# Optimization experiments

Measured on AMD Instinct MI355X. Metric: run time of the kernel, lower is better.

## Reference

```python
import jax, jax.numpy as jnp
import numpy as np

NUM_HEADS = 8
WINDOW = 7
DILATION = 1
EPS = 1e-5


def channel_ln(x, w, b):
    # x: [B, C, H, W]; normalize over channel dim (axis=1)
    mu = jnp.mean(x, axis=1, keepdims=True)
    var = jnp.var(x, axis=1, keepdims=True)
    xhat = (x - mu) * jax.lax.rsqrt(var + EPS)
    return xhat * w[None, :, None, None] + b[None, :, None, None]


def local_mask(H, W, window, dilation):
    r = (window // 2) * dilation
    ii, jj = jnp.meshgrid(jnp.arange(H), jnp.arange(W), indexing="ij")
    ii = ii.reshape(-1)
    jj = jj.reshape(-1)
    di = jnp.abs(ii[:, None] - ii[None, :])
    dj = jnp.abs(jj[:, None] - jj[None, :])
    m = (di <= r) & (dj <= r)
    if dilation > 1:
        m = m & (di % dilation == 0) & (dj % dilation == 0)
    return m  # [N, N] bool


def local_attention(x, qkv_w, qkv_b, proj_w, proj_b):
    B, C, H, W = x.shape
    N = H * W
    hd = C // NUM_HEADS
    t = x.reshape(B, C, N).transpose(0, 2, 1)            # [B, N, C]
    qkv = t @ qkv_w.T + qkv_b                            # [B, N, 3C]
    qkv = qkv.reshape(B, N, 3, NUM_HEADS, hd)
    q, k, v = (qkv[:, :, i].transpose(0, 2, 1, 3) for i in range(3))  # [B,h,N,d]
    scale = 1.0 / jnp.sqrt(jnp.asarray(hd, x.dtype))
    scores = jnp.einsum("bhnd,bhmd->bhnm", q, k) * scale  # [B,h,N,N]
    mask = local_mask(H, W, WINDOW, DILATION)             # [N,N]
    scores = jnp.where(mask[None, None], scores, jnp.asarray(-jnp.inf, x.dtype))
    attn = jax.nn.softmax(scores, axis=-1)
    out = jnp.einsum("bhnm,bhmd->bhnd", attn, v)          # [B,h,N,d]
    out = out.transpose(0, 2, 1, 3).reshape(B, N, C)      # [B,N,C]
    out = out @ proj_w.T + proj_b
    return out.transpose(0, 2, 1).reshape(B, C, H, W)


def mlp2d(x, fc1_w, fc1_b, fc2_w, fc2_b):
    # 1x1 convs == per-pixel linear over channels
    h = jnp.einsum("bchw,oc->bohw", x, fc1_w) + fc1_b[None, :, None, None]
    h = jax.nn.gelu(h, approximate=False)
    return jnp.einsum("bchw,oc->bohw", h, fc2_w) + fc2_b[None, :, None, None]


def setup_inputs() -> dict:
    key = jax.random.key(0)
    ks = jax.random.split(key, 12)
    B, C, H, W = 1, 256, 56, 56
    hidden = 4 * C
    s = lambda fan: 1.0 / np.sqrt(fan)
    return {
        "x": jax.random.normal(ks[0], (B, C, H, W), jnp.float32),
        "norm1_w": jnp.ones((C,), jnp.float32),
        "norm1_b": jnp.zeros((C,), jnp.float32),
        "qkv_w": jax.random.normal(ks[1], (3 * C, C), jnp.float32) * s(C),
        "qkv_b": jnp.zeros((3 * C,), jnp.float32),
        "proj_w": jax.random.normal(ks[2], (C, C), jnp.float32) * s(C),
        "proj_b": jnp.zeros((C,), jnp.float32),
        "norm2_w": jnp.ones((C,), jnp.float32),
        "norm2_b": jnp.zeros((C,), jnp.float32),
        "fc1_w": jax.random.normal(ks[3], (hidden, C), jnp.float32) * s(C),
        "fc1_b": jnp.zeros((hidden,), jnp.float32),
        "fc2_w": jax.random.normal(ks[4], (C, hidden), jnp.float32) * s(hidden),
        "fc2_b": jnp.zeros((C,), jnp.float32),
    }


def reference(x, norm1_w, norm1_b, qkv_w, qkv_b, proj_w, proj_b,
              norm2_w, norm2_b, fc1_w, fc1_b, fc2_w, fc2_b):
    x = x + local_attention(channel_ln(x, norm1_w, norm1_b), qkv_w, qkv_b, proj_w, proj_b)
    x = x + mlp2d(channel_ln(x, norm2_w, norm2_b), fc1_w, fc1_b, fc2_w, fc2_b)
    return x
```

## Files before the change

### kernel.cpp

```cpp
#include <hip/hip_runtime.h>
#include <math.h>


typedef unsigned int uint;
typedef unsigned short ushort;
typedef unsigned long long u64;
typedef __attribute__((ext_vector_type(8))) short short8;
typedef __attribute__((ext_vector_type(4))) float floatx4;
typedef __attribute__((ext_vector_type(4))) unsigned short ushort4v;

#define AS1(p) (const __attribute__((address_space(1))) void*)(p)
#define AS3(p) (__attribute__((address_space(3))) void*)(p)

__device__ __forceinline__ float bf2f(ushort u) {
  union { uint i; float f; } v; v.i = ((uint)u) << 16; return v.f;
}
__device__ __forceinline__ ushort f2bf(float f) {
  union { float f; uint i; } v; v.f = f;
  uint u = v.i;
  return (ushort)((u + 0x7fffu + ((u >> 16) & 1u)) >> 16);
}

__device__ __forceinline__ void stage64(const ushort* src, int kstride,
                                        ushort* dstBase, int tid) {
  const int srow = tid >> 5;
  const int scb  = (tid & 31) ^ srow;
  const ushort* g = src + (size_t)srow * kstride + scb * 8;
  ushort* d = dstBase + tid * 8;
  #pragma unroll
  for (int r = 0; r < 8; ++r) {
    __builtin_amdgcn_global_load_lds(AS1(g), AS3(d), 16, 0, 0);
    g += 8 * kstride;
    d += 2048;
  }
}

__device__ __forceinline__ void compute64(const ushort* As, const ushort* Bs,
                                          int w, int lane, floatx4 acc[4]) {
  const int fm = lane & 15;
  const int q  = lane >> 4;
  const int swz = fm & 7;
  const int arow = (w * 16 + fm) * 256;
  #pragma unroll
  for (int kt = 0; kt < 8; ++kt) {
    const int blk = ((kt * 4 + q) ^ swz) * 8;
    short8 af = *(const short8*)&As[arow + blk];
    #pragma unroll
    for (int nt = 0; nt < 4; ++nt) {
      short8 bfr = *(const short8*)&Bs[(nt * 16 + fm) * 256 + blk];
      acc[nt] = __builtin_amdgcn_mfma_f32_16x16x32_bf16(af, bfr, acc[nt], 0, 0, 0);
    }
  }
}

__global__ __launch_bounds__(256) void prep_kernel(
    const float* __restrict__ x, const float* __restrict__ n1w,
    const float* __restrict__ n1b,
    const float* __restrict__ qkvw, const float* __restrict__ projw,
    const float* __restrict__ f1w, const float* __restrict__ f2w,
    float* __restrict__ xT, ushort* __restrict__ t1, ushort* __restrict__ wcat)
{
  const int tid = threadIdx.x;
  const int bid = blockIdx.x;
  if (bid >= 196) {
    int idx = (bid - 196) * 256 + tid;
    float v;
    if (idx < 196608)       v = qkvw[idx];
    else if (idx < 262144)  v = projw[idx - 196608];
    else if (idx < 524288)  v = f1w[idx - 262144];
    else                    v = f2w[idx - 524288];
    wcat[idx] = f2bf(v);
    return;
  }
  __shared__ float tile[256 * 17];
  __shared__ float red[2][16][16];
  __shared__ float mu[16], rsv[16];
  const int n0 = bid * 16;
  const int px = tid & 15, grp = tid >> 4;
  #pragma unroll 4
  for (int it = 0; it < 16; ++it) {
    int c = it * 16 + grp;
    tile[c * 17 + px] = x[(size_t)c * 3136 + n0 + px];
  }
  __syncthreads();
  float s = 0.f, ss = 0.f;
  #pragma unroll
  for (int i = 0; i < 16; ++i) {
    float v = tile[(grp * 16 + i) * 17 + px];
    s += v; ss += v * v;
  }
  red[0][px][grp] = s; red[1][px][grp] = ss;
  __syncthreads();
  if (tid < 16) {
    float s2 = 0.f, ss2 = 0.f;
    #pragma unroll
    for (int g = 0; g < 16; ++g) { s2 += red[0][tid][g]; ss2 += red[1][tid][g]; }
    float m = s2 * (1.f / 256.f);
    float var = ss2 * (1.f / 256.f) - m * m;
    mu[tid] = m;
    rsv[tid] = rsqrtf(var + 1e-5f);
  }
  __syncthreads();
  const float wc = n1w[tid], bc = n1b[tid];
  #pragma unroll 4
  for (int p = 0; p < 16; ++p) {
    float v = tile[tid * 17 + p];
    xT[(size_t)(n0 + p) * 256 + tid] = v;
    t1[(size_t)(n0 + p) * 256 + tid] = f2bf((v - mu[p]) * rsv[p] * wc + bc);
  }
}

__global__ __launch_bounds__(256, 2) void qkv_kernel(
    const ushort* __restrict__ A, const ushort* __restrict__ B,
    const float* __restrict__ bias, ushort* __restrict__ out)
{
  __shared__ ushort As[16384], Bs[16384];
  const int tid = threadIdx.x, lane = tid & 63, w = tid >> 6;
  const int m0 = blockIdx.y * 64, n0 = blockIdx.x * 64;
  floatx4 acc[4] = {{0.f,0.f,0.f,0.f},{0.f,0.f,0.f,0.f},
                    {0.f,0.f,0.f,0.f},{0.f,0.f,0.f,0.f}};
  stage64(A + (size_t)m0 * 256, 256, As, tid);
  stage64(B + (size_t)n0 * 256, 256, Bs, tid);
  asm volatile("s_waitcnt vmcnt(0)" ::: "memory");
  __syncthreads();
  compute64(As, Bs, w, lane, acc);
  const int fm = lane & 15, q4 = (lane >> 4) * 4;
  #pragma unroll
  for (int nt = 0; nt < 4; ++nt)
    #pragma unroll
    for (int r = 0; r < 4; ++r) {
      int m = m0 + w * 16 + q4 + r;
      int n = n0 + nt * 16 + fm;
      float v = acc[nt][r] + bias[n];
      if (n < 256) v *= 0.17677669529663687f;
      out[(size_t)m * 768 + n] = f2bf(v);
    }
}

__global__ __launch_bounds__(256, 1) void attn_kernel(
    const ushort* __restrict__ qkv, ushort* __restrict__ out)
{
  __shared__ ushort Kh[100 * 260];
  __shared__ ushort Vh[100 * 256];
  __shared__ float pr[16 * 8 * 64];
  const int tid = threadIdx.x;
  const int i0 = (blockIdx.x / 14) * 4, j0 = (blockIdx.x % 14) * 4;

  for (int s = tid; s < 3200; s += 256) {
    int p = s >> 5, ck = s & 31;
    int ii = i0 - 3 + p / 10, jj = j0 - 3 + p % 10;
    if (ii >= 0 && ii < 56 && jj >= 0 && jj < 56) {
      const ushort* kr = qkv + (size_t)(ii * 56 + jj) * 768 + 256 + ck * 8;
      short8 kv = *(const short8*)kr;
      u64 lo = ((const u64*)&kv)[0], hi = ((const u64*)&kv)[1];
      *(u64*)&Kh[p * 260 + ck * 8] = lo;
      *(u64*)&Kh[p * 260 + ck * 8 + 4] = hi;
      *(short8*)&Vh[p * 256 + ck * 8] = *(const short8*)(kr + 256);
    } else {
      *(u64*)&Kh[p * 260 + ck * 8] = 0ull;
      *(u64*)&Kh[p * 260 + ck * 8 + 4] = 0ull;
      short8 z = {0, 0, 0, 0, 0, 0, 0, 0};
      *(short8*)&Vh[p * 256 + ck * 8] = z;
    }
  }
  __syncthreads();

  const int wv = tid >> 6, lane = tid & 63;
  const int h = lane >> 3, mg = lane & 7;
  for (int qq = 0; qq < 4; ++qq) {
    const int p = wv * 4 + qq;
    const int qi = p >> 2, qj = p & 3;
    const int iq = i0 + qi, jq = j0 + qj;
    const ushort* qp = qkv + (size_t)(iq * 56 + jq) * 768 + h * 32;
    float qf[32];
    #pragma unroll
    for (int u = 0; u < 4; ++u) {
      short8 qv = *(const short8*)(qp + u * 8);
      #pragma unroll
      for (int e = 0; e < 8; ++e) qf[u * 8 + e] = bf2f((ushort)qv[e]);
    }
    float sv[7];
    float mx = -1e30f;
    #pragma unroll
    for (int k = 0; k < 7; ++k) {
      int m = mg + 8 * k;
      float s = -1e30f;
      if (m < 49) {
        int mi = m / 7, mj = m % 7;
        int ii = iq + mi - 3, jj = jq + mj - 3;
        if (ii >= 0 && ii < 56 && jj >= 0 && jj < 56) {
          int hrow = (qi + mi) * 10 + (qj + mj);
          const u64* k8 = (const u64*)&Kh[hrow * 260 + h * 32];
          float a = 0.f;
          #pragma unroll
          for (int u = 0; u < 8; ++u) {
            u64 kv = k8[u];
            #pragma unroll
            for (int e = 0; e < 4; ++e)
              a += qf[u * 4 + e] * bf2f((ushort)(kv >> (16 * e)));
          }
          s = a;
        }
      }
      sv[k] = s;
      mx = fmaxf(mx, s);
    }
    mx = fmaxf(mx, __shfl_xor(mx, 1));
    mx = fmaxf(mx, __shfl_xor(mx, 2));
    mx = fmaxf(mx, __shfl_xor(mx, 4));
    float sm = 0.f;
    #pragma unroll
    for (int k = 0; k < 7; ++k) { sv[k] = __expf(sv[k] - mx); sm += sv[k]; }
    sm += __shfl_xor(sm, 1);
    sm += __shfl_xor(sm, 2);
    sm += __shfl_xor(sm, 4);
    float inv = 1.f / sm;
    #pragma unroll
    for (int k = 0; k < 7; ++k) {
      int m = mg + 8 * k;
      pr[(p * 8 + h) * 64 + m] = sv[k] * inv;
    }
  }
  __syncthreads();

  const int qsel = tid >> 5, cg = tid & 31, hh = cg >> 2;
  #pragma unroll
  for (int pass = 0; pass < 2; ++pass) {
    const int p = pass * 8 + qsel;
    const int qi = p >> 2, qj = p & 3;
    float acc8[8] = {0, 0, 0, 0, 0, 0, 0, 0};
    #pragma unroll
    for (int mi = 0; mi < 7; ++mi)
      #pragma unroll
      for (int mj = 0; mj < 7; ++mj) {
        int m = mi * 7 + mj;
        int hrow = (qi + mi) * 10 + (qj + mj);
        float pm = pr[(p * 8 + hh) * 64 + m];
        short8 v8 = *(const short8*)&Vh[hrow * 256 + cg * 8];
        #pragma unroll
        for (int e = 0; e < 8; ++e)
          acc8[e] += pm * bf2f((ushort)v8[e]);
      }
    const int n = (i0 + qi) * 56 + (j0 + qj);
    short8 o;
    #pragma unroll
    for (int e = 0; e < 8; ++e) o[e] = (short)f2bf(acc8[e]);
    *(short8*)&out[(size_t)n * 256 + cg * 8] = o;
  }
}

__global__ __launch_bounds__(256, 2) void proj_kernel(
    const ushort* __restrict__ A, const ushort* __restrict__ B,
    const float* __restrict__ bias, const float* __restrict__ resid,
    float* __restrict__ x1)
{
  __shared__ ushort As[16384], Bs[16384];
  const int tid = threadIdx.x, lane = tid & 63, w = tid >> 6;
  const int m0 = blockIdx.y * 64, n0 = blockIdx.x * 64;
  floatx4 acc[4] = {{0.f,0.f,0.f,0.f},{0.f,0.f,0.f,0.f},
                    {0.f,0.f,0.f,0.f},{0.f,0.f,0.f,0.f}};
  stage64(A + (size_t)m0 * 256, 256, As, tid);
  stage64(B + (size_t)n0 * 256, 256, Bs, tid);
  asm volatile("s_waitcnt vmcnt(0)" ::: "memory");
  __syncthreads();
  compute64(As, Bs, w, lane, acc);
  const int fm = lane & 15, q4 = (lane >> 4) * 4;
  #pragma unroll
  for (int nt = 0; nt < 4; ++nt)
    #pragma unroll
    for (int r = 0; r < 4; ++r) {
      int m = m0 + w * 16 + q4 + r;
      int n = n0 + nt * 16 + fm;
      x1[(size_t)m * 256 + n] = acc[nt][r] + bias[n] + resid[(size_t)m * 256 + n];
    }
}

__global__ __launch_bounds__(256, 2) void fc1_kernel(
    const float* __restrict__ x1, const ushort* __restrict__ B,
    const float* __restrict__ n2w, const float* __restrict__ n2b,
    const float* __restrict__ bias, ushort* __restrict__ out)
{
  __shared__ ushort As[16384], Bs[16384];
  __shared__ float stats[128];
  const int tid = threadIdx.x, lane = tid & 63, w = tid >> 6;
  const int m0 = blockIdx.y * 64, n0 = blockIdx.x * 64;

  stage64(B + (size_t)n0 * 256, 256, Bs, tid);

  {
    const int r = tid >> 2, seg = tid & 3;
    const float* src = x1 + (size_t)(m0 + r) * 256 + seg * 64;
    float s = 0.f, ss = 0.f;
    #pragma unroll
    for (int i = 0; i < 16; ++i) {
      floatx4 v = *(const floatx4*)(src + i * 4);
      s += v[0] + v[1] + v[2] + v[3];
      ss += v[0]*v[0] + v[1]*v[1] + v[2]*v[2] + v[3]*v[3];
    }
    s += __shfl_xor(s, 1); ss += __shfl_xor(ss, 1);
    s += __shfl_xor(s, 2); ss += __shfl_xor(ss, 2);
    if (seg == 0) {
      float mu = s * (1.f / 256.f);
      float var = ss * (1.f / 256.f) - mu * mu;
      stats[r * 2] = mu;
      stats[r * 2 + 1] = rsqrtf(var + 1e-5f);
    }
  }
  __syncthreads();
  #pragma unroll
  for (int k = 0; k < 8; ++k) {
    int s = tid + k * 256;
    int row = s >> 5, cb = s & 31;
    int gb = cb ^ (row & 7);
    float mu = stats[row * 2], rs = stats[row * 2 + 1];
    const float* src = x1 + (size_t)(m0 + row) * 256 + gb * 8;
    floatx4 a = *(const floatx4*)(src);
    floatx4 b2 = *(const floatx4*)(src + 4);
    floatx4 w1 = *(const floatx4*)(n2w + gb * 8);
    floatx4 w2 = *(const floatx4*)(n2w + gb * 8 + 4);
    floatx4 b1v = *(const floatx4*)(n2b + gb * 8);
    floatx4 b2v = *(const floatx4*)(n2b + gb * 8 + 4);
    short8 o;
    #pragma unroll
    for (int e = 0; e < 4; ++e) {
      o[e]     = (short)f2bf((a[e]  - mu) * rs * w1[e] + b1v[e]);
      o[e + 4] = (short)f2bf((b2[e] - mu) * rs * w2[e] + b2v[e]);
    }
    *(short8*)&As[row * 256 + cb * 8] = o;
  }
  asm volatile("s_waitcnt vmcnt(0)" ::: "memory");
  __syncthreads();

  floatx4 acc[4] = {{0.f,0.f,0.f,0.f},{0.f,0.f,0.f,0.f},
                    {0.f,0.f,0.f,0.f},{0.f,0.f,0.f,0.f}};
  compute64(As, Bs, w, lane, acc);
  const int fm = lane & 15, q4 = (lane >> 4) * 4;
  #pragma unroll
  for (int nt = 0; nt < 4; ++nt)
    #pragma unroll
    for (int r = 0; r < 4; ++r) {
      int m = m0 + w * 16 + q4 + r;
      int n = n0 + nt * 16 + fm;
      float v = acc[nt][r] + bias[n];
      v = 0.5f * v * (1.0f + erff(v * 0.70710678118654752f));
      out[(size_t)m * 1024 + n] = f2bf(v);
    }
}

__global__ __launch_bounds__(256, 2) void fc2_kernel(
    const ushort* __restrict__ A, const ushort* __restrict__ B,
    const float* __restrict__ bias, const float* __restrict__ x1,
    float* __restrict__ outf)
{
  __shared__ ushort As[16384], Bs[16384];
  const int tid = threadIdx.x, lane = tid & 63, w = tid >> 6;
  const int m0 = blockIdx.y * 64, n0 = blockIdx.x * 64;
  floatx4 acc[4] = {{0.f,0.f,0.f,0.f},{0.f,0.f,0.f,0.f},
                    {0.f,0.f,0.f,0.f},{0.f,0.f,0.f,0.f}};
  for (int kc = 0; kc < 4; ++kc) {
    if (kc) __syncthreads();
    stage64(A + (size_t)m0 * 1024 + kc * 256, 1024, As, tid);
    stage64(B + (size_t)n0 * 1024 + kc * 256, 1024, Bs, tid);
    asm volatile("s_waitcnt vmcnt(0)" ::: "memory");
    __syncthreads();
    compute64(As, Bs, w, lane, acc);
  }
  const int fm = lane & 15, q4 = (lane >> 4) * 4;
  #pragma unroll
  for (int nt = 0; nt < 4; ++nt)
    #pragma unroll
    for (int r = 0; r < 4; ++r) {
      int m = m0 + w * 16 + q4 + r;
      int n = n0 + nt * 16 + fm;
      outf[(size_t)m * 3136 + n] = acc[nt][r] + bias[m] + x1[(size_t)n * 256 + m];
    }
}

extern "C" void kernel_launch(void* const* d_in, const int* in_sizes, int n_in,
                              void* d_out, int out_size, void* d_ws, size_t ws_size,
                              hipStream_t stream) {
  const float* x     = (const float*)d_in[0];
  const float* n1w   = (const float*)d_in[1];
  const float* n1b   = (const float*)d_in[2];
  const float* qkvw  = (const float*)d_in[3];
  const float* qkvb  = (const float*)d_in[4];
  const float* projw = (const float*)d_in[5];
  const float* projb = (const float*)d_in[6];
  const float* n2w   = (const float*)d_in[7];
  const float* n2b   = (const float*)d_in[8];
  const float* f1w   = (const float*)d_in[9];
  const float* f1b   = (const float*)d_in[10];
  const float* f2w   = (const float*)d_in[11];
  const float* f2b   = (const float*)d_in[12];

  char* ws = (char*)d_ws;
  ushort* wcat = (ushort*)(ws + 0);
  float*  xT   = (float*)(ws + 1572864);
  ushort* t    = (ushort*)(ws + 4784128);
  ushort* qh   = (ushort*)(ws + 6389760);
  ushort* attnO= (ushort*)(ws + 12812288);

  const ushort* qw_bf = wcat;
  const ushort* pw_bf = wcat + 196608;
  const ushort* f1_bf = wcat + 262144;
  const ushort* f2_bf = wcat + 524288;
  float* outf = (float*)d_out;

  hipLaunchKernelGGL(prep_kernel, dim3(3268), dim3(256), 0, stream,
                     x, n1w, n1b, qkvw, projw, f1w, f2w, xT, t, wcat);
  hipLaunchKernelGGL(qkv_kernel, dim3(12, 49), dim3(256), 0, stream,
                     t, qw_bf, qkvb, qh);
  hipLaunchKernelGGL(attn_kernel, dim3(196), dim3(256), 0, stream, qh, attnO);
  hipLaunchKernelGGL(proj_kernel, dim3(4, 49), dim3(256), 0, stream,
                     attnO, pw_bf, projb, xT, xT);
  hipLaunchKernelGGL(fc1_kernel, dim3(16, 49), dim3(256), 0, stream,
                     xT, f1_bf, n2w, n2b, f1b, qh);
  hipLaunchKernelGGL(fc2_kernel, dim3(49, 4), dim3(256), 0, stream,
                     f2_bf, qh, f2b, xT, outf);
}
```

Baseline: 147.0 us.

## Fuse output projection and residual add into the local attention kernel

The attention kernel now keeps its 16-query by 256-channel output tile in shared memory and applies the output projection directly. It streams the projection weights through double-buffered shared-memory chunks that reuse the dead K and probability regions, then does MFMA plus bias and residual add. This removes the separate proj launch and the global write and read of the attention output. The cost is that every block now reads the full projection weight matrix for only 16 rows, which adds L2 traffic. The result also goes to a new x1 buffer instead of being written back into xT.

```diff
diff --git a/kernel.cpp b/kernel.cpp
--- a/kernel.cpp
+++ b/kernel.cpp
@@ -137,12 +137,21 @@
     }
 }
 
-__global__ __launch_bounds__(256, 1) void attn_kernel(
-    const ushort* __restrict__ qkv, ushort* __restrict__ out)
+#define ATTN_SMEM 144416
+
+__global__ __launch_bounds__(256, 1) void attnproj_kernel(
+    const ushort* __restrict__ qkv, const ushort* __restrict__ pw_bf,
+    const float* __restrict__ projb, const float* __restrict__ xT,
+    float* __restrict__ x1)
 {
-  __shared__ ushort Kh[100 * 260];
-  __shared__ ushort Vh[100 * 256];
-  __shared__ float pr[16 * 8 * 64];
+  __shared__ __align__(16) char smem[ATTN_SMEM];
+  ushort* Kh  = (ushort*)smem;
+  ushort* Vh  = (ushort*)(smem + 52000);
+  float*  pr  = (float*)(smem + 103200);
+  ushort* aas = (ushort*)(smem + 135968);
+  ushort* Bs0 = (ushort*)smem;
+  ushort* Bs1 = (ushort*)(smem + 103200);
+
   const int tid = threadIdx.x;
   const int i0 = (blockIdx.x / 14) * 4, j0 = (blockIdx.x % 14) * 4;
 
@@ -223,56 +232,62 @@
   }
   __syncthreads();
 
-  const int qsel = tid >> 5, cg = tid & 31, hh = cg >> 2;
-  #pragma unroll
-  for (int pass = 0; pass < 2; ++pass) {
-    const int p = pass * 8 + qsel;
-    const int qi = p >> 2, qj = p & 3;
-    float acc8[8] = {0, 0, 0, 0, 0, 0, 0, 0};
-    #pragma unroll
-    for (int mi = 0; mi < 7; ++mi)
+  stage64(pw_bf, 256, Bs0, tid);
+
+  {
+    const int qsel = tid >> 5, cg = tid & 31, hh = cg >> 2;
+    #pragma unroll
+    for (int pass = 0; pass < 2; ++pass) {
+      const int p = pass * 8 + qsel;
+      const int qi = p >> 2, qj = p & 3;
+      float acc8[8] = {0, 0, 0, 0, 0, 0, 0, 0};
       #pragma unroll
-      for (int mj = 0; mj < 7; ++mj) {
-        int m = mi * 7 + mj;
-        int hrow = (qi + mi) * 10 + (qj + mj);
-        float pm = pr[(p * 8 + hh) * 64 + m];
-        short8 v8 = *(const short8*)&Vh[hrow * 256 + cg * 8];
+      for (int mi = 0; mi < 7; ++mi)
         #pragma unroll
-        for (int e = 0; e < 8; ++e)
-          acc8[e] += pm * bf2f((ushort)v8[e]);
-      }
-    const int n = (i0 + qi) * 56 + (j0 + qj);
-    short8 o;
-    #pragma unroll
-    for (int e = 0; e < 8; ++e) o[e] = (short)f2bf(acc8[e]);
-    *(short8*)&out[(size_t)n * 256 + cg * 8] = o;
-  }
-}
-
-__global__ __launch_bounds__(256, 2) void proj_kernel(
-    const ushort* __restrict__ A, const ushort* __restrict__ B,
-    const float* __restrict__ bias, const float* __restrict__ resid,
-    float* __restrict__ x1)
-{
-  __shared__ ushort As[16384], Bs[16384];
-  const int tid = threadIdx.x, lane = tid & 63, w = tid >> 6;
-  const int m0 = blockIdx.y * 64, n0 = blockIdx.x * 64;
-  floatx4 acc[4] = {{0.f,0.f,0.f,0.f},{0.f,0.f,0.f,0.f},
-                    {0.f,0.f,0.f,0.f},{0.f,0.f,0.f,0.f}};
-  stage64(A + (size_t)m0 * 256, 256, As, tid);
-  stage64(B + (size_t)n0 * 256, 256, Bs, tid);
-  asm volatile("s_waitcnt vmcnt(0)" ::: "memory");
-  __syncthreads();
-  compute64(As, Bs, w, lane, acc);
-  const int fm = lane & 15, q4 = (lane >> 4) * 4;
-  #pragma unroll
-  for (int nt = 0; nt < 4; ++nt)
+        for (int mj = 0; mj < 7; ++mj) {
+          int m = mi * 7 + mj;
+          int hrow = (qi + mi) * 10 + (qj + mj);
+          float pm = pr[(p * 8 + hh) * 64 + m];
+          short8 v8 = *(const short8*)&Vh[hrow * 256 + cg * 8];
+          #pragma unroll
+          for (int e = 0; e < 8; ++e)
+            acc8[e] += pm * bf2f((ushort)v8[e]);
+        }
+      short8 o;
+      #pragma unroll
+      for (int e = 0; e < 8; ++e) o[e] = (short)f2bf(acc8[e]);
+      *(short8*)&aas[p * 264 + cg * 8] = o;
+    }
+  }
+  __syncthreads();
+
+  const int fm = lane & 15, q = lane >> 4, q4 = q * 4;
+  for (int c = 0; c < 4; ++c) {
+    if (c > 0) __syncthreads();
+    if (c < 3) {
+      stage64(pw_bf + (size_t)(c + 1) * 64 * 256, 256, (c & 1) ? Bs0 : Bs1, tid);
+      asm volatile("s_waitcnt vmcnt(8)" ::: "memory");
+    } else {
+      asm volatile("s_waitcnt vmcnt(0)" ::: "memory");
+    }
+    __syncthreads();
+    const ushort* Bc = (c & 1) ? Bs1 : Bs0;
+    floatx4 acc = {0.f, 0.f, 0.f, 0.f};
+    const int rr = wv * 16 + fm;
+    #pragma unroll
+    for (int kt = 0; kt < 8; ++kt) {
+      short8 af = *(const short8*)&aas[fm * 264 + kt * 32 + q * 8];
+      short8 bfr = *(const short8*)&Bc[rr * 256 + (((kt * 4 + q) ^ (fm & 7))) * 8];
+      acc = __builtin_amdgcn_mfma_f32_16x16x32_bf16(af, bfr, acc, 0, 0, 0);
+    }
+    const int ch = c * 64 + wv * 16 + fm;
     #pragma unroll
     for (int r = 0; r < 4; ++r) {
-      int m = m0 + w * 16 + q4 + r;
-      int n = n0 + nt * 16 + fm;
-      x1[(size_t)m * 256 + n] = acc[nt][r] + bias[n] + resid[(size_t)m * 256 + n];
-    }
+      int p = q4 + r;
+      int n = (i0 + (p >> 2)) * 56 + j0 + (p & 3);
+      x1[(size_t)n * 256 + ch] = acc[r] + projb[ch] + xT[(size_t)n * 256 + ch];
+    }
+  }
 }
 
 __global__ __launch_bounds__(256, 2) void fc1_kernel(
@@ -398,7 +413,7 @@
   float*  xT   = (float*)(ws + 1572864);
   ushort* t    = (ushort*)(ws + 4784128);
   ushort* qh   = (ushort*)(ws + 6389760);
-  ushort* attnO= (ushort*)(ws + 12812288);
+  float*  x1   = (float*)(ws + 12812288);
 
   const ushort* qw_bf = wcat;
   const ushort* pw_bf = wcat + 196608;
@@ -410,11 +425,10 @@
                      x, n1w, n1b, qkvw, projw, f1w, f2w, xT, t, wcat);
   hipLaunchKernelGGL(qkv_kernel, dim3(12, 49), dim3(256), 0, stream,
                      t, qw_bf, qkvb, qh);
-  hipLaunchKernelGGL(attn_kernel, dim3(196), dim3(256), 0, stream, qh, attnO);
-  hipLaunchKernelGGL(proj_kernel, dim3(4, 49), dim3(256), 0, stream,
-                     attnO, pw_bf, projb, xT, xT);
+  hipLaunchKernelGGL(attnproj_kernel, dim3(196), dim3(256), 0, stream,
+                     qh, pw_bf, projb, xT, x1);
   hipLaunchKernelGGL(fc1_kernel, dim3(16, 49), dim3(256), 0, stream,
-                     xT, f1_bf, n2w, n2b, f1b, qh);
+                     x1, f1_bf, n2w, n2b, f1b, qh);
   hipLaunchKernelGGL(fc2_kernel, dim3(49, 4), dim3(256), 0, stream,
-                     f2_bf, qh, f2b, xT, outf);
-}
+                     f2_bf, qh, f2b, x1, outf);
+}
```

Result: no change. 147.5 us (+0.3%).
